# Kernel optimization log

Hardware: AMD Instinct MI355X
Metric: run time of the kernel (lower is better)

Reference implementation:

```python
import jax, jax.numpy as jnp
import numpy as np

N_NODES = 50000


def gcn_norm(edge_index, edge_weight, n):
    """PyG GCNConv normalization: add self-loops (weight 1), sym-normalize."""
    src, dst = edge_index[0], edge_index[1]
    loop = jnp.arange(n, dtype=src.dtype)
    src = jnp.concatenate([src, loop])
    dst = jnp.concatenate([dst, loop])
    w = jnp.concatenate([edge_weight, jnp.ones((n,), dtype=edge_weight.dtype)])
    deg = jax.ops.segment_sum(w, dst, num_segments=n)  # in-degree w/ self-loops
    dis = jnp.where(deg > 0, jax.lax.rsqrt(deg), 0.0)  # deg^{-1/2}, inf -> 0
    norm = dis[src] * w * dis[dst]                      # [E+N]
    return src, dst, norm


def gcn_conv(x, src, dst, norm, W, b):
    h = x @ W                                            # [N, F_out]
    msg = norm[:, None] * h[src]                         # gather + scale
    out = jax.ops.segment_sum(msg, dst, num_segments=x.shape[0])  # scatter-add
    return out + b


def setup_inputs() -> dict:
    key = jax.random.key(0)
    ks = jax.random.split(key, 10)
    n, e = N_NODES, 800000
    in_dim, hidden, out_dim = 256, 128, 64
    x = jax.random.normal(ks[0], (n, in_dim), dtype=jnp.float32)
    edge_index = jax.random.randint(ks[1], (2, e), 0, n, dtype=jnp.int32)
    edge_weight = jax.random.uniform(ks[2], (e,), dtype=jnp.float32)
    def glorot(k, fi, fo):
        lim = float(np.sqrt(6.0 / (fi + fo)))
        return jax.random.uniform(k, (fi, fo), minval=-lim, maxval=lim, dtype=jnp.float32)
    return {
        "x": x, "edge_index": edge_index, "edge_weight": edge_weight,
        "W1": glorot(ks[3], in_dim, hidden), "b1": jnp.zeros((hidden,), jnp.float32),
        "W2": glorot(ks[4], hidden, hidden), "b2": jnp.zeros((hidden,), jnp.float32),
        "W3": glorot(ks[5], hidden, out_dim), "b3": jnp.zeros((out_dim,), jnp.float32),
    }


def reference(x, edge_index, edge_weight, W1, b1, W2, b2, W3, b3):
    n = x.shape[0]
    src, dst, norm = gcn_norm(edge_index, edge_weight, n)  # cached=True: shared
    h = jax.nn.relu(gcn_conv(x, src, dst, norm, W1, b1))   # dropout: eval mode no-op
    h = jax.nn.relu(gcn_conv(h, src, dst, norm, W2, b2))
    h = gcn_conv(h, src, dst, norm, W3, b3)
    return h
```

## Files before the change

### kernel.cpp

```cpp
#include <hip/hip_runtime.h>
#include <hip/hip_bf16.h>
#include <stdint.h>

#define NODES 50000
#define EDGES 800000

#define EPB 4096
#define NBLK ((EDGES + EPB - 1) / EPB)
#define NBUK ((NODES + 63) / 64)
#define NBUKP 1024
#define CAP 2560

#define NVB_GEMM ((NODES / 16 + 3) / 4)

typedef short bf16x8 __attribute__((ext_vector_type(8)));
typedef float f32x4 __attribute__((ext_vector_type(4)));

__device__ __forceinline__ unsigned short f2bf(float f) {
    union { float f; unsigned u; } v; v.f = f;
    unsigned r = v.u + 0x7fff + ((v.u >> 16) & 1);
    return (unsigned short)(r >> 16);
}
__device__ __forceinline__ float bf2f(unsigned short h) {
    union { float f; unsigned u; } v; v.u = ((unsigned)h) << 16;
    return v.f;
}
__device__ __forceinline__ float bflo(unsigned hv) {
    union { float f; unsigned u; } v; v.u = hv << 16;
    return v.f;
}
__device__ __forceinline__ float bfhi(unsigned hv) {
    union { float f; unsigned u; } v; v.u = hv & 0xffff0000u;
    return v.f;
}

__device__ __forceinline__ void wfrag_one(const float* __restrict__ W, unsigned short* Wf,
                                          int idx, int K, int Nn) {
    int NT = Nn >> 4;
    int lane = idx & 63;
    int f = idx >> 6;
    int nt = f % NT;
    int k0 = (f / NT) << 5;
    int n = (nt << 4) + (lane & 15);
    int kk = k0 + ((lane >> 4) << 3);
    unsigned short o[8];
#pragma unroll
    for (int j = 0; j < 8; j++) o[j] = f2bf(W[(kk + j) * Nn + n]);
    ((uint4*)Wf)[idx] = *(uint4*)o;
}

__global__ void k_setup_hist(const int* __restrict__ dst, unsigned* __restrict__ hist,
                             int* __restrict__ cursor,
                             const float* __restrict__ W1, unsigned short* Wf1,
                             const float* __restrict__ W2, unsigned short* Wf2,
                             const float* __restrict__ W3, unsigned short* Wf3) {
    if ((int)blockIdx.x < NBLK) {
        __shared__ unsigned cnt[NBUK];
        int t = threadIdx.x;
        for (int i = t; i < NBUK; i += 256) cnt[i] = 0;
        __syncthreads();
        int base = blockIdx.x * EPB;
#pragma unroll
        for (int i = 0; i < EPB / 256; i++) {
            int e = base + i * 256 + t;
            if (e < EDGES) atomicAdd(&cnt[((unsigned)dst[e]) >> 6], 1u);
        }
        __syncthreads();
        for (int b = t; b < NBUK; b += 256) hist[b * NBLK + blockIdx.x] = cnt[b];
    } else {
        int idx = (blockIdx.x - NBLK) * 256 + threadIdx.x;
        if (idx == 0) *cursor = 0;
        if (idx < 4096) wfrag_one(W1, Wf1, idx, 256, 128);
        else if (idx < 6144) wfrag_one(W2, Wf2, idx - 4096, 128, 128);
        else if (idx < 7168) wfrag_one(W3, Wf3, idx - 6144, 128, 64);
    }
}

__global__ void k_hscan(unsigned* __restrict__ hist, int2* __restrict__ brange,
                        int* __restrict__ cursor) {
    __shared__ int sm[256];
    __shared__ int s_base;
    int b = blockIdx.x, t = threadIdx.x;
    int v = (t < NBLK) ? (int)hist[b * NBLK + t] : 0;
    sm[t] = v;
    __syncthreads();
    for (int off = 1; off < 256; off <<= 1) {
        int x2 = (t >= off) ? sm[t - off] : 0;
        __syncthreads();
        sm[t] += x2;
        __syncthreads();
    }
    int total = sm[255];
    if (t == 0) s_base = atomicAdd(cursor, total);
    __syncthreads();
    if (t < NBLK) hist[b * NBLK + t] = (unsigned)(s_base + sm[t] - v);
    if (t == 0) { int2 r; r.x = s_base; r.y = total; brange[b] = r; }
}

template <int K, int Nn, bool A_F32>
__device__ __forceinline__ void gemm_vb(const void* __restrict__ A_,
                                        const uint4* __restrict__ Wf,
                                        unsigned short* __restrict__ Hout, int vb) {
    constexpr int NT = Nn / 16;
    int lane = threadIdx.x & 63;
    int wave = threadIdx.x >> 6;
    int tile = vb * 4 + wave;
    if (tile * 16 >= NODES) return;
    int row = tile * 16 + (lane & 15);
    int kbase = (lane >> 4) * 8;

    f32x4 acc[NT];
#pragma unroll
    for (int i = 0; i < NT; i++) acc[i] = (f32x4){0.f, 0.f, 0.f, 0.f};

    for (int k0 = 0; k0 < K; k0 += 32) {
        bf16x8 a;
        if (A_F32) {
            const float* A = (const float*)A_;
            const float4* pp = (const float4*)&A[(size_t)row * K + k0 + kbase];
            float4 u0 = pp[0], u1 = pp[1];
            unsigned short t[8];
            t[0] = f2bf(u0.x); t[1] = f2bf(u0.y); t[2] = f2bf(u0.z); t[3] = f2bf(u0.w);
            t[4] = f2bf(u1.x); t[5] = f2bf(u1.y); t[6] = f2bf(u1.z); t[7] = f2bf(u1.w);
            a = *(bf16x8*)t;
        } else {
            const unsigned short* A = (const unsigned short*)A_;
            a = *(const bf16x8*)&A[(size_t)row * K + k0 + kbase];
        }
        int fbase = (k0 >> 5) * NT;
#pragma unroll
        for (int nt = 0; nt < NT; nt++) {
            uint4 braw = Wf[(fbase + nt) * 64 + lane];
            bf16x8 b = *(bf16x8*)&braw;
            acc[nt] = __builtin_amdgcn_mfma_f32_16x16x32_bf16(a, b, acc[nt], 0, 0, 0);
        }
    }
    int r0 = (lane >> 4) * 4;
    int col = lane & 15;
#pragma unroll
    for (int nt = 0; nt < NT; nt++) {
#pragma unroll
        for (int r = 0; r < 4; r++) {
            int m = tile * 16 + r0 + r;
            Hout[(size_t)m * Nn + nt * 16 + col] = f2bf(acc[nt][r]);
        }
    }
}

__global__ void k_sort_gemm1(const int* __restrict__ src, const int* __restrict__ dst,
                             const float* __restrict__ w, const unsigned* __restrict__ gbase,
                             int2* __restrict__ rec,
                             const float* __restrict__ x, const uint4* __restrict__ Wf1,
                             unsigned short* __restrict__ h) {
    __shared__ unsigned long long rec_lds[EPB];
    __shared__ unsigned cnt[NBUKP];
    __shared__ unsigned lst[NBUKP];
    __shared__ unsigned gb[NBUK];
    __shared__ int part[256];

    int blk = blockIdx.x;
    if (blk >= NBLK) {
        gemm_vb<256, 128, true>((const void*)x, Wf1, h, blk - NBLK);
        return;
    }
    int t = threadIdx.x;
    for (int b = t; b < NBUK; b += 256) gb[b] = gbase[b * NBLK + blk];
    for (int b = t; b < NBUKP; b += 256) cnt[b] = 0;
    __syncthreads();

    int base = blk * EPB;
    int nrec = EDGES - base; if (nrec > EPB) nrec = EPB;

#pragma unroll
    for (int i = 0; i < EPB / 256; i++) {
        int e = base + i * 256 + t;
        if (e < EDGES) atomicAdd(&cnt[((unsigned)dst[e]) >> 6], 1u);
    }
    __syncthreads();

    unsigned s0 = cnt[t * 4], s1 = cnt[t * 4 + 1], s2 = cnt[t * 4 + 2], s3 = cnt[t * 4 + 3];
    unsigned ps = s0 + s1 + s2 + s3;
    part[t] = (int)ps;
    __syncthreads();
    for (int off = 1; off < 256; off <<= 1) {
        int x2 = (t >= off) ? part[t - off] : 0;
        __syncthreads();
        part[t] += x2;
        __syncthreads();
    }
    unsigned excl = (unsigned)part[t] - ps;
    lst[t * 4] = excl;
    lst[t * 4 + 1] = excl + s0;
    lst[t * 4 + 2] = excl + s0 + s1;
    lst[t * 4 + 3] = excl + s0 + s1 + s2;
    __syncthreads();
    for (int b = t; b < NBUKP; b += 256) cnt[b] = 0;
    __syncthreads();

#pragma unroll
    for (int i = 0; i < EPB / 256; i++) {
        int e = base + i * 256 + t;
        if (e < EDGES) {
            unsigned d = (unsigned)dst[e];
            unsigned b = d >> 6;
            unsigned r = atomicAdd(&cnt[b], 1u);
            unsigned meta = (unsigned)src[e] | ((d & 63u) << 16) | (b << 22);
            unsigned long long v = (unsigned long long)meta |
                                   ((unsigned long long)__float_as_uint(w[e]) << 32);
            rec_lds[lst[b] + r] = v;
        }
    }
    __syncthreads();

    for (int i = t; i < nrec; i += 256) {
        unsigned long long v = rec_lds[i];
        unsigned meta = (unsigned)v;
        unsigned b = meta >> 22;
        unsigned gpos = gb[b] + ((unsigned)i - lst[b]);
        int2 rc; rc.x = (int)(meta & 0x3FFFFFu); rc.y = (int)(v >> 32);
        rec[gpos] = rc;
    }
}

__global__ void k_sub(int2* __restrict__ rec, const int2* __restrict__ brange,
                      float* __restrict__ dis, int2* __restrict__ rsc) {
    __shared__ int2 stage[CAP];
    __shared__ unsigned short ipos[CAP];
    __shared__ unsigned cnt[64];
    __shared__ unsigned lst[64];
    __shared__ float degw[64];
    int t = threadIdx.x, b = blockIdx.x;
    int2 br = brange[b];
    int base = br.x;
    int n = br.y; if (n > CAP) n = CAP;

    if (t < 64) { cnt[t] = 0; degw[t] = 0.f; }
    __syncthreads();
    for (int i = t; i < n; i += 256) {
        int2 rc = rec[base + i];
        stage[i] = rc;
        unsigned dl = ((unsigned)rc.x >> 16) & 63u;
        atomicAdd(&cnt[dl], 1u);
        atomicAdd(&degw[dl], __int_as_float(rc.y));
    }
    __syncthreads();
    if (t == 0) {
        unsigned run = 0;
        for (int j = 0; j < 64; j++) { lst[j] = run; run += cnt[j]; }
    }
    __syncthreads();
    if (t < 64) {
        int node = b * 64 + t;
        if (node < NODES) {
            dis[node] = rsqrtf(1.0f + degw[t]);
            int2 rs; rs.x = base + (int)lst[t]; rs.y = (int)cnt[t];
            rsc[node] = rs;
        }
    }
    if (t < 64) cnt[t] = 0;
    __syncthreads();
    for (int i = t; i < n; i += 256) {
        unsigned dl = ((unsigned)stage[i].x >> 16) & 63u;
        unsigned r = atomicAdd(&cnt[dl], 1u);
        ipos[lst[dl] + r] = (unsigned short)i;
    }
    __syncthreads();
    for (int i = t; i < n; i += 256) {
        rec[base + i] = stage[ipos[i]];
    }
}

template <int K, int Nn, bool A_F32>
__global__ void k_gemm(const void* __restrict__ A_, const uint4* __restrict__ Wf,
                       unsigned short* __restrict__ Hout) {
    gemm_vb<K, Nn, A_F32>(A_, Wf, Hout, blockIdx.x);
}

template <int F, bool RELU, bool OUT_F32>
__global__ void k_agg(const unsigned short* __restrict__ H, const int2* __restrict__ rec,
                      const int2* __restrict__ rsc, const float* __restrict__ dis,
                      const float* __restrict__ bias, void* __restrict__ out_) {
    constexpr int VPT = F / 64;
    int lane = threadIdx.x & 63;
    int node = blockIdx.x * 4 + (threadIdx.x >> 6);
    if (node >= NODES) return;
    node = __builtin_amdgcn_readfirstlane(node);

    const unsigned* H32 = (const unsigned*)H;

    float dn = dis[node];
    float acc0, acc1 = 0.f;
    if (VPT == 2) {
        unsigned hv = H32[node * 64 + lane];
        acc0 = dn * bflo(hv);
        acc1 = dn * bfhi(hv);
    } else {
        acc0 = dn * bf2f(H[node * 64 + lane]);
    }

    int2 rs = rsc[node];
    int beg = rs.x, end = rs.x + rs.y;
    int last = end - 1;
    for (int j = beg; j < end; j += 8) {
        int ss[8]; float nn[8];
#pragma unroll
        for (int q = 0; q < 8; q++) {
            int idx = j + q;
            idx = (idx < last) ? idx : last;
            int2 rc = rec[idx];
            ss[q] = rc.x & 0xFFFF;
            nn[q] = (j + q < end) ? __int_as_float(rc.y) : 0.0f;
        }
#pragma unroll
        for (int q = 0; q < 8; q++) nn[q] *= dis[ss[q]];
        if (VPT == 2) {
            unsigned hh[8];
#pragma unroll
            for (int q = 0; q < 8; q++) hh[q] = H32[ss[q] * 64 + lane];
#pragma unroll
            for (int q = 0; q < 8; q++) {
                acc0 += nn[q] * bflo(hh[q]);
                acc1 += nn[q] * bfhi(hh[q]);
            }
        } else {
            unsigned short hh[8];
#pragma unroll
            for (int q = 0; q < 8; q++) hh[q] = H[ss[q] * 64 + lane];
#pragma unroll
            for (int q = 0; q < 8; q++) acc0 += nn[q] * bf2f(hh[q]);
        }
    }

    if (OUT_F32) {
        float* out = (float*)out_;
        if (VPT == 2) {
            float x0 = dn * acc0 + bias[lane * 2];
            float x1 = dn * acc1 + bias[lane * 2 + 1];
            if (RELU) { x0 = fmaxf(x0, 0.f); x1 = fmaxf(x1, 0.f); }
            out[(size_t)node * F + lane * 2] = x0;
            out[(size_t)node * F + lane * 2 + 1] = x1;
        } else {
            float x0 = dn * acc0 + bias[lane];
            if (RELU) x0 = fmaxf(x0, 0.f);
            out[(size_t)node * F + lane] = x0;
        }
    } else {
        unsigned short* out = (unsigned short*)out_;
        if (VPT == 2) {
            float x0 = dn * acc0 + bias[lane * 2];
            float x1 = dn * acc1 + bias[lane * 2 + 1];
            if (RELU) { x0 = fmaxf(x0, 0.f); x1 = fmaxf(x1, 0.f); }
            unsigned pk = (unsigned)f2bf(x0) | ((unsigned)f2bf(x1) << 16);
            *(unsigned*)&out[(size_t)node * F + lane * 2] = pk;
        } else {
            float x0 = dn * acc0 + bias[lane];
            if (RELU) x0 = fmaxf(x0, 0.f);
            out[(size_t)node * F + lane] = f2bf(x0);
        }
    }
}


extern "C" void kernel_launch(void* const* d_in, const int* in_sizes, int n_in,
                              void* d_out, int out_size, void* d_ws, size_t ws_size,
                              hipStream_t stream) {
    const float* x  = (const float*)d_in[0];
    const int*   ei = (const int*)d_in[1];
    const float* w  = (const float*)d_in[2];
    const float* W1 = (const float*)d_in[3];
    const float* b1 = (const float*)d_in[4];
    const float* W2 = (const float*)d_in[5];
    const float* b2 = (const float*)d_in[6];
    const float* W3 = (const float*)d_in[7];
    const float* b3 = (const float*)d_in[8];
    const int* src = ei;
    const int* dst = ei + EDGES;

    char* p = (char*)d_ws;
    auto alloc = [&](size_t n) { char* r = p; p += (n + 511) & ~(size_t)511; return r; };
    unsigned*       hist   = (unsigned*)alloc((size_t)NBUK * NBLK * 4);
    int2*           brange = (int2*)alloc((size_t)NBUK * 8);
    int*            cursor = (int*)alloc(4);
    int2*           rec    = (int2*)alloc((size_t)EDGES * 8);
    float*          dis    = (float*)alloc(NODES * 4);
    int2*           rsc    = (int2*)alloc((size_t)NODES * 8);
    unsigned short* h      = (unsigned short*)alloc((size_t)NODES * 128 * 2);
    unsigned short* xb     = (unsigned short*)alloc((size_t)NODES * 128 * 2);
    unsigned short* wf1    = (unsigned short*)alloc(256 * 128 * 2);
    unsigned short* wf2    = (unsigned short*)alloc(128 * 128 * 2);
    unsigned short* wf3    = (unsigned short*)alloc(128 * 64 * 2);

    const int TB = 256;

    hipLaunchKernelGGL(k_setup_hist, dim3(NBLK + 28), dim3(TB), 0, stream,
                       dst, hist, cursor, W1, wf1, W2, wf2, W3, wf3);
    hipLaunchKernelGGL(k_hscan, dim3(NBUK), dim3(TB), 0, stream, hist, brange, cursor);
    hipLaunchKernelGGL(k_sort_gemm1, dim3(NBLK + NVB_GEMM), dim3(TB), 0, stream,
                       src, dst, w, hist, rec, x, (const uint4*)wf1, h);
    hipLaunchKernelGGL(k_sub, dim3(NBUK), dim3(TB), 0, stream, rec, brange, dis, rsc);

    int nb_gemm = NVB_GEMM;
    int nb_agg  = (NODES + 3) / 4;

    hipLaunchKernelGGL((k_agg<128, true, false>), dim3(nb_agg), dim3(TB), 0, stream, h, rec, rsc, dis, b1, (void*)xb);

    hipLaunchKernelGGL((k_gemm<128, 128, false>), dim3(nb_gemm), dim3(TB), 0, stream, (const void*)xb, (const uint4*)wf2, h);
    hipLaunchKernelGGL((k_agg<128, true, false>), dim3(nb_agg), dim3(TB), 0, stream, h, rec, rsc, dis, b2, (void*)xb);

    hipLaunchKernelGGL((k_gemm<128, 64, false>), dim3(nb_gemm), dim3(TB), 0, stream, (const void*)xb, (const uint4*)wf3, h);
    hipLaunchKernelGGL((k_agg<64, false, true>), dim3(nb_agg), dim3(TB), 0, stream, h, rec, rsc, dis, b3, d_out);
}
```

Measured before the change: 304.2 us.

## Rework sort/GEMM1 fusion, transpose MFMA output stores, split aggregation across half-waves

The sort and first-GEMM kernel now runs 1024-thread blocks and interleaves sort blocks with GEMM blocks, so each GEMM block handles 16 tiles and each sort block scans 1024 buckets in a single pass. The MFMA operands are swapped so each lane holds consecutive output columns, which allows packed 8-byte stores instead of scalar 2-byte stores. The aggregation kernel has each half-wave process alternate neighbours with wider vector loads and combines the halves with a shuffle at the end. The aim is better memory coalescing and more loads in flight, at the cost of higher register and LDS pressure in the big blocks. Interleaving also assumes the GEMM tiles (NGB) fit within NBLK.

```diff
diff --git a/kernel.cpp b/kernel.cpp
--- a/kernel.cpp
+++ b/kernel.cpp
@@ -11,7 +11,8 @@
 #define NBUKP 1024
 #define CAP 2560
 
-#define NVB_GEMM ((NODES / 16 + 3) / 4)
+#define NTILE (NODES / 16)
+#define NGB ((NTILE + 15) / 16)
 
 typedef short bf16x8 __attribute__((ext_vector_type(8)));
 typedef float f32x4 __attribute__((ext_vector_type(4)));
@@ -20,10 +21,6 @@
     union { float f; unsigned u; } v; v.f = f;
     unsigned r = v.u + 0x7fff + ((v.u >> 16) & 1);
     return (unsigned short)(r >> 16);
-}
-__device__ __forceinline__ float bf2f(unsigned short h) {
-    union { float f; unsigned u; } v; v.u = ((unsigned)h) << 16;
-    return v.f;
 }
 __device__ __forceinline__ float bflo(unsigned hv) {
     union { float f; unsigned u; } v; v.u = hv << 16;
@@ -98,13 +95,11 @@
 }
 
 template <int K, int Nn, bool A_F32>
-__device__ __forceinline__ void gemm_vb(const void* __restrict__ A_,
-                                        const uint4* __restrict__ Wf,
-                                        unsigned short* __restrict__ Hout, int vb) {
+__device__ __forceinline__ void gemm_tile(const void* __restrict__ A_,
+                                          const uint4* __restrict__ Wf,
+                                          unsigned short* __restrict__ Hout, int tile) {
     constexpr int NT = Nn / 16;
     int lane = threadIdx.x & 63;
-    int wave = threadIdx.x >> 6;
-    int tile = vb * 4 + wave;
     if (tile * 16 >= NODES) return;
     int row = tile * 16 + (lane & 15);
     int kbase = (lane >> 4) * 8;
@@ -132,92 +127,86 @@
         for (int nt = 0; nt < NT; nt++) {
             uint4 braw = Wf[(fbase + nt) * 64 + lane];
             bf16x8 b = *(bf16x8*)&braw;
-            acc[nt] = __builtin_amdgcn_mfma_f32_16x16x32_bf16(a, b, acc[nt], 0, 0, 0);
-        }
-    }
-    int r0 = (lane >> 4) * 4;
-    int col = lane & 15;
+            acc[nt] = __builtin_amdgcn_mfma_f32_16x16x32_bf16(b, a, acc[nt], 0, 0, 0);
+        }
+    }
+    int xr = lane & 15;
+    int wg = lane >> 4;
 #pragma unroll
     for (int nt = 0; nt < NT; nt++) {
-#pragma unroll
-        for (int r = 0; r < 4; r++) {
-            int m = tile * 16 + r0 + r;
-            Hout[(size_t)m * Nn + nt * 16 + col] = f2bf(acc[nt][r]);
-        }
-    }
-}
-
-__global__ void k_sort_gemm1(const int* __restrict__ src, const int* __restrict__ dst,
-                             const float* __restrict__ w, const unsigned* __restrict__ gbase,
-                             int2* __restrict__ rec,
-                             const float* __restrict__ x, const uint4* __restrict__ Wf1,
-                             unsigned short* __restrict__ h) {
+        uint2 pk;
+        pk.x = (unsigned)f2bf(acc[nt][0]) | ((unsigned)f2bf(acc[nt][1]) << 16);
+        pk.y = (unsigned)f2bf(acc[nt][2]) | ((unsigned)f2bf(acc[nt][3]) << 16);
+        ((uint2*)Hout)[(((size_t)(tile * 16 + xr) * Nn + nt * 16) >> 2) + wg] = pk;
+    }
+}
+
+__global__ __launch_bounds__(1024) void
+k_sort_gemm1(const int* __restrict__ src, const int* __restrict__ dst,
+             const float* __restrict__ w, const unsigned* __restrict__ gbase,
+             int2* __restrict__ rec,
+             const float* __restrict__ x, const uint4* __restrict__ Wf1,
+             unsigned short* __restrict__ h) {
     __shared__ unsigned long long rec_lds[EPB];
     __shared__ unsigned cnt[NBUKP];
     __shared__ unsigned lst[NBUKP];
     __shared__ unsigned gb[NBUK];
-    __shared__ int part[256];
+    __shared__ int sm[1024];
 
     int blk = blockIdx.x;
-    if (blk >= NBLK) {
-        gemm_vb<256, 128, true>((const void*)x, Wf1, h, blk - NBLK);
+    int t = threadIdx.x;
+    if (blk & 1) {
+        gemm_tile<256, 128, true>((const void*)x, Wf1, h, (blk >> 1) * 16 + (t >> 6));
         return;
     }
-    int t = threadIdx.x;
-    for (int b = t; b < NBUK; b += 256) gb[b] = gbase[b * NBLK + blk];
-    for (int b = t; b < NBUKP; b += 256) cnt[b] = 0;
-    __syncthreads();
-
-    int base = blk * EPB;
+    int sb = blk >> 1;
+    if (t < NBUK) gb[t] = gbase[t * NBLK + sb];
+    cnt[t] = 0;
+    __syncthreads();
+
+    int base = sb * EPB;
     int nrec = EDGES - base; if (nrec > EPB) nrec = EPB;
 
 #pragma unroll
-    for (int i = 0; i < EPB / 256; i++) {
-        int e = base + i * 256 + t;
+    for (int i = 0; i < EPB / 1024; i++) {
+        int e = base + i * 1024 + t;
         if (e < EDGES) atomicAdd(&cnt[((unsigned)dst[e]) >> 6], 1u);
     }
     __syncthreads();
 
-    unsigned s0 = cnt[t * 4], s1 = cnt[t * 4 + 1], s2 = cnt[t * 4 + 2], s3 = cnt[t * 4 + 3];
-    unsigned ps = s0 + s1 + s2 + s3;
-    part[t] = (int)ps;
-    __syncthreads();
-    for (int off = 1; off < 256; off <<= 1) {
-        int x2 = (t >= off) ? part[t - off] : 0;
-        __syncthreads();
-        part[t] += x2;
-        __syncthreads();
-    }
-    unsigned excl = (unsigned)part[t] - ps;
-    lst[t * 4] = excl;
-    lst[t * 4 + 1] = excl + s0;
-    lst[t * 4 + 2] = excl + s0 + s1;
-    lst[t * 4 + 3] = excl + s0 + s1 + s2;
-    __syncthreads();
-    for (int b = t; b < NBUKP; b += 256) cnt[b] = 0;
-    __syncthreads();
-
-#pragma unroll
-    for (int i = 0; i < EPB / 256; i++) {
-        int e = base + i * 256 + t;
+    int v = (int)cnt[t];
+    sm[t] = v;
+    __syncthreads();
+    for (int off = 1; off < 1024; off <<= 1) {
+        int x2 = (t >= off) ? sm[t - off] : 0;
+        __syncthreads();
+        sm[t] += x2;
+        __syncthreads();
+    }
+    lst[t] = (unsigned)(sm[t] - v);
+    cnt[t] = 0;
+    __syncthreads();
+
+#pragma unroll
+    for (int i = 0; i < EPB / 1024; i++) {
+        int e = base + i * 1024 + t;
         if (e < EDGES) {
             unsigned d = (unsigned)dst[e];
             unsigned b = d >> 6;
             unsigned r = atomicAdd(&cnt[b], 1u);
             unsigned meta = (unsigned)src[e] | ((d & 63u) << 16) | (b << 22);
-            unsigned long long v = (unsigned long long)meta |
-                                   ((unsigned long long)__float_as_uint(w[e]) << 32);
-            rec_lds[lst[b] + r] = v;
-        }
-    }
-    __syncthreads();
-
-    for (int i = t; i < nrec; i += 256) {
-        unsigned long long v = rec_lds[i];
-        unsigned meta = (unsigned)v;
+            rec_lds[lst[b] + r] = (unsigned long long)meta |
+                                  ((unsigned long long)__float_as_uint(w[e]) << 32);
+        }
+    }
+    __syncthreads();
+
+    for (int i = t; i < nrec; i += 1024) {
+        unsigned long long vv = rec_lds[i];
+        unsigned meta = (unsigned)vv;
         unsigned b = meta >> 22;
         unsigned gpos = gb[b] + ((unsigned)i - lst[b]);
-        int2 rc; rc.x = (int)(meta & 0x3FFFFFu); rc.y = (int)(v >> 32);
+        int2 rc; rc.x = (int)(meta & 0x3FFFFFu); rc.y = (int)(vv >> 32);
         rec[gpos] = rc;
     }
 }
@@ -273,30 +262,33 @@
 template <int K, int Nn, bool A_F32>
 __global__ void k_gemm(const void* __restrict__ A_, const uint4* __restrict__ Wf,
                        unsigned short* __restrict__ Hout) {
-    gemm_vb<K, Nn, A_F32>(A_, Wf, Hout, blockIdx.x);
+    gemm_tile<K, Nn, A_F32>(A_, Wf, Hout, blockIdx.x * 4 + (threadIdx.x >> 6));
 }
 
 template <int F, bool RELU, bool OUT_F32>
 __global__ void k_agg(const unsigned short* __restrict__ H, const int2* __restrict__ rec,
                       const int2* __restrict__ rsc, const float* __restrict__ dis,
                       const float* __restrict__ bias, void* __restrict__ out_) {
-    constexpr int VPT = F / 64;
+    constexpr int CPL = F / 32;
     int lane = threadIdx.x & 63;
+    int l5 = lane & 31;
+    int hf = lane >> 5;
     int node = blockIdx.x * 4 + (threadIdx.x >> 6);
     if (node >= NODES) return;
     node = __builtin_amdgcn_readfirstlane(node);
 
-    const unsigned* H32 = (const unsigned*)H;
-
     float dn = dis[node];
-    float acc0, acc1 = 0.f;
-    if (VPT == 2) {
-        unsigned hv = H32[node * 64 + lane];
-        acc0 = dn * bflo(hv);
-        acc1 = dn * bfhi(hv);
+    float acc[CPL];
+    if (CPL == 4) {
+        uint2 hv = ((const uint2*)H)[(size_t)node * 32 + l5];
+        acc[0] = bflo(hv.x); acc[1] = bfhi(hv.x);
+        acc[2] = bflo(hv.y); acc[3] = bfhi(hv.y);
     } else {
-        acc0 = dn * bf2f(H[node * 64 + lane]);
-    }
+        unsigned hv = ((const unsigned*)H)[(size_t)node * 32 + l5];
+        acc[0] = bflo(hv); acc[1] = bfhi(hv);
+    }
+#pragma unroll
+    for (int j = 0; j < CPL; j++) acc[j] = hf ? 0.f : dn * acc[j];
 
     int2 rs = rsc[node];
     int beg = rs.x, end = rs.x + rs.y;
@@ -313,49 +305,53 @@
         }
 #pragma unroll
         for (int q = 0; q < 8; q++) nn[q] *= dis[ss[q]];
-        if (VPT == 2) {
-            unsigned hh[8];
-#pragma unroll
-            for (int q = 0; q < 8; q++) hh[q] = H32[ss[q] * 64 + lane];
-#pragma unroll
-            for (int q = 0; q < 8; q++) {
-                acc0 += nn[q] * bflo(hh[q]);
-                acc1 += nn[q] * bfhi(hh[q]);
+#pragma unroll
+        for (int pj = 0; pj < 4; pj++) {
+            int srow = hf ? ss[2 * pj + 1] : ss[2 * pj];
+            float nw = hf ? nn[2 * pj + 1] : nn[2 * pj];
+            if (CPL == 4) {
+                uint2 hv = ((const uint2*)H)[(size_t)srow * 32 + l5];
+                acc[0] += nw * bflo(hv.x); acc[1] += nw * bfhi(hv.x);
+                acc[2] += nw * bflo(hv.y); acc[3] += nw * bfhi(hv.y);
+            } else {
+                unsigned hv = ((const unsigned*)H)[(size_t)srow * 32 + l5];
+                acc[0] += nw * bflo(hv); acc[1] += nw * bfhi(hv);
+            }
+        }
+    }
+#pragma unroll
+    for (int j = 0; j < CPL; j++) acc[j] += __shfl_xor(acc[j], 32);
+
+    if (hf == 0) {
+        if (CPL == 4) {
+            float x0 = dn * acc[0] + bias[l5 * 4 + 0];
+            float x1 = dn * acc[1] + bias[l5 * 4 + 1];
+            float x2 = dn * acc[2] + bias[l5 * 4 + 2];
+            float x3 = dn * acc[3] + bias[l5 * 4 + 3];
+            if (RELU) {
+                x0 = fmaxf(x0, 0.f); x1 = fmaxf(x1, 0.f);
+                x2 = fmaxf(x2, 0.f); x3 = fmaxf(x3, 0.f);
+            }
+            if (OUT_F32) {
+                float4 o; o.x = x0; o.y = x1; o.z = x2; o.w = x3;
+                ((float4*)out_)[(size_t)node * 32 + l5] = o;
+            } else {
+                uint2 pk;
+                pk.x = (unsigned)f2bf(x0) | ((unsigned)f2bf(x1) << 16);
+                pk.y = (unsigned)f2bf(x2) | ((unsigned)f2bf(x3) << 16);
+                ((uint2*)out_)[(size_t)node * 32 + l5] = pk;
             }
         } else {
-            unsigned short hh[8];
-#pragma unroll
-            for (int q = 0; q < 8; q++) hh[q] = H[ss[q] * 64 + lane];
-#pragma unroll
-            for (int q = 0; q < 8; q++) acc0 += nn[q] * bf2f(hh[q]);
-        }
-    }
-
-    if (OUT_F32) {
-        float* out = (float*)out_;
-        if (VPT == 2) {
-            float x0 = dn * acc0 + bias[lane * 2];
-            float x1 = dn * acc1 + bias[lane * 2 + 1];
+            float x0 = dn * acc[0] + bias[l5 * 2 + 0];
+            float x1 = dn * acc[1] + bias[l5 * 2 + 1];
             if (RELU) { x0 = fmaxf(x0, 0.f); x1 = fmaxf(x1, 0.f); }
-            out[(size_t)node * F + lane * 2] = x0;
-            out[(size_t)node * F + lane * 2 + 1] = x1;
-        } else {
-            float x0 = dn * acc0 + bias[lane];
-            if (RELU) x0 = fmaxf(x0, 0.f);
-            out[(size_t)node * F + lane] = x0;
-        }
-    } else {
-        unsigned short* out = (unsigned short*)out_;
-        if (VPT == 2) {
-            float x0 = dn * acc0 + bias[lane * 2];
-            float x1 = dn * acc1 + bias[lane * 2 + 1];
-            if (RELU) { x0 = fmaxf(x0, 0.f); x1 = fmaxf(x1, 0.f); }
-            unsigned pk = (unsigned)f2bf(x0) | ((unsigned)f2bf(x1) << 16);
-            *(unsigned*)&out[(size_t)node * F + lane * 2] = pk;
-        } else {
-            float x0 = dn * acc0 + bias[lane];
-            if (RELU) x0 = fmaxf(x0, 0.f);
-            out[(size_t)node * F + lane] = f2bf(x0);
+            if (OUT_F32) {
+                float2 o; o.x = x0; o.y = x1;
+                ((float2*)out_)[(size_t)node * 32 + l5] = o;
+            } else {
+                unsigned pk = (unsigned)f2bf(x0) | ((unsigned)f2bf(x1) << 16);
+                ((unsigned*)out_)[(size_t)node * 32 + l5] = pk;
+            }
         }
     }
 }
@@ -395,11 +391,11 @@
     hipLaunchKernelGGL(k_setup_hist, dim3(NBLK + 28), dim3(TB), 0, stream,
                        dst, hist, cursor, W1, wf1, W2, wf2, W3, wf3);
     hipLaunchKernelGGL(k_hscan, dim3(NBUK), dim3(TB), 0, stream, hist, brange, cursor);
-    hipLaunchKernelGGL(k_sort_gemm1, dim3(NBLK + NVB_GEMM), dim3(TB), 0, stream,
+    hipLaunchKernelGGL(k_sort_gemm1, dim3(2 * NBLK), dim3(1024), 0, stream,
                        src, dst, w, hist, rec, x, (const uint4*)wf1, h);
     hipLaunchKernelGGL(k_sub, dim3(NBUK), dim3(TB), 0, stream, rec, brange, dis, rsc);
 
-    int nb_gemm = NVB_GEMM;
+    int nb_gemm = (NTILE + 3) / 4;
     int nb_agg  = (NODES + 3) / 4;
 
     hipLaunchKernelGGL((k_agg<128, true, false>), dim3(nb_agg), dim3(TB), 0, stream, h, rec, rsc, dis, b1, (void*)xb);
```

After: 1.036 ms. 241% more time.
